# Performance work log

Measured on AMD Instinct MI355X. Metric: run time of the kernel, lower is better.

The kernel has to match this reference:

```python
import jax, jax.numpy as jnp
import numpy as np


def _ln(x, g, b, eps=1e-6):
    m = jnp.mean(x, axis=-1, keepdims=True)
    v = jnp.var(x, axis=-1, keepdims=True)
    return (x - m) * jax.lax.rsqrt(v + eps) * g + b


def setup_inputs():
    key = jax.random.key(0)
    ks = jax.random.split(key, 16)
    B, Hs, Ws, D = 2, 48, 48, 768
    heads, P = 6, 4
    L = Hs * Ws                # feat tokens (single level, 1/16 scale)
    N = 21 * (Hs * Ws // 4)    # query tokens: 16n + 4n + n multi-scale layout
    hidden = int(D * 0.25)
    s = 0.02
    return {
        "query": jax.random.normal(ks[0], (B, N, D), jnp.float32),
        "reference_points": jax.random.uniform(ks[1], (B, N, 1, 2), jnp.float32),
        "feat": jax.random.normal(ks[2], (B, L, D), jnp.float32),
        "spatial_shapes": jnp.array([[Hs, Ws]], jnp.int32),
        "level_start_index": jnp.array([0], jnp.int32),
        "H": Hs, "W": Ws,
        "qn_g": jnp.ones((D,), jnp.float32), "qn_b": jnp.zeros((D,), jnp.float32),
        "fn_g": jnp.ones((D,), jnp.float32), "fn_b": jnp.zeros((D,), jnp.float32),
        "Wv": jax.random.normal(ks[3], (D, D), jnp.float32) * s, "bv": jnp.zeros((D,), jnp.float32),
        "Woff": jax.random.normal(ks[4], (D, heads * P * 2), jnp.float32) * s,
        "boff": jax.random.normal(ks[5], (heads * P * 2,), jnp.float32) * s,
        "Wattn": jax.random.normal(ks[6], (D, heads * P), jnp.float32) * s,
        "battn": jnp.zeros((heads * P,), jnp.float32),
        "Wo": jax.random.normal(ks[7], (D, D), jnp.float32) * s, "bo": jnp.zeros((D,), jnp.float32),
        "ffn_g": jnp.ones((D,), jnp.float32), "ffn_b": jnp.zeros((D,), jnp.float32),
        "W1": jax.random.normal(ks[8], (D, hidden), jnp.float32) * s, "b1": jnp.zeros((hidden,), jnp.float32),
        "dw_w": jax.random.normal(ks[9], (hidden, 1, 3, 3), jnp.float32) * s, "dw_b": jnp.zeros((hidden,), jnp.float32),
        "W2": jax.random.normal(ks[10], (hidden, D), jnp.float32) * s, "b2": jnp.zeros((D,), jnp.float32),
    }


def reference(query, reference_points, feat, spatial_shapes, level_start_index, H, W,
              qn_g, qn_b, fn_g, fn_b, Wv, bv, Woff, boff, Wattn, battn, Wo, bo,
              ffn_g, ffn_b, W1, b1, dw_w, dw_b, W2, b2):
    B, N, D = query.shape
    heads, P = 6, 4
    dh = D // heads
    hidden = W1.shape[1]
    # ---- MSDeformAttn (single level) ----
    qn = _ln(query, qn_g, qn_b)
    fn = _ln(feat, fn_g, fn_b)
    value = (fn @ Wv + bv).reshape(B, -1, heads, dh)           # (B,L,h,dh)
    off = (qn @ Woff + boff).reshape(B, N, heads, 1, P, 2)
    aw = jax.nn.softmax((qn @ Wattn + battn).reshape(B, N, heads, P), axis=-1)
    # offset normalizer = [W_l, H_l]
    norm = jnp.stack([spatial_shapes[..., 1], spatial_shapes[..., 0]], -1).astype(qn.dtype)
    loc = reference_points[:, :, None, :, None, :] + off / norm[None, None, None, :, None, :]
    loc = loc[:, :, :, 0]  # (B,N,heads,P,2) single level
    # grid_sample bilinear, align_corners=False, zero padding
    x = loc[..., 0] * W - 0.5
    y = loc[..., 1] * H - 0.5
    x0 = jnp.floor(x); y0 = jnp.floor(y)
    wx = x - x0; wy = y - y0
    x0 = x0.astype(jnp.int32); y0 = y0.astype(jnp.int32)
    value_t = value.transpose(0, 2, 1, 3)  # (B,heads,L,dh)

    def corner(xi, yi, w):
        valid = (xi >= 0) & (xi < W) & (yi >= 0) & (yi < H)
        idx = jnp.clip(yi, 0, H - 1) * W + jnp.clip(xi, 0, W - 1)
        idx = idx.transpose(0, 2, 1, 3).reshape(B, heads, N * P)
        v = jnp.take_along_axis(value_t, idx[..., None], axis=2)  # (B,h,N*P,dh)
        wm = jnp.where(valid, w, 0.0).transpose(0, 2, 1, 3).reshape(B, heads, N * P)
        return v * wm[..., None]

    sampled = (corner(x0, y0, (1 - wx) * (1 - wy)) + corner(x0 + 1, y0, wx * (1 - wy))
               + corner(x0, y0 + 1, (1 - wx) * wy) + corner(x0 + 1, y0 + 1, wx * wy))
    sampled = sampled.reshape(B, heads, N, P, dh)
    attn = jnp.einsum('bhnpd,bnhp->bnhd', sampled, aw).reshape(B, N, D) @ Wo + bo
    query = query + attn
    # ---- ConvFFN (hidden=dim*cffn_ratio, multi-scale DWConv) ----
    h = _ln(query, ffn_g, ffn_b) @ W1 + b1
    n = N // 21

    def dw(t, hh, ww):
        img = t.transpose(0, 2, 1).reshape(B, hidden, hh, ww)
        out = jax.lax.conv_general_dilated(img, dw_w, (1, 1), 'SAME', feature_group_count=hidden)
        return (out + dw_b[None, :, None, None]).reshape(B, hidden, hh * ww).transpose(0, 2, 1)

    h = jnp.concatenate([dw(h[:, :16 * n], 2 * H, 2 * W),
                         dw(h[:, 16 * n:20 * n], H, W),
                         dw(h[:, 20 * n:], H // 2, W // 2)], axis=1)
    h = jax.nn.gelu(h, approximate=False)
    return query + (h @ W2 + b2)
```

## Files before the change

kernel.cpp:

```cpp
#include <hip/hip_runtime.h>
#include <math.h>

#define BB 2
#define NN 12096
#define LL 2304
#define DD 768
#define HID 192
#define HS 48
#define WS 48

typedef unsigned short u16;
typedef unsigned int u32;
typedef __attribute__((ext_vector_type(8))) __bf16 bf16x8;
typedef __attribute__((ext_vector_type(4))) float f32x4;

__device__ __forceinline__ u16 f2bf(float f) {
  u32 x = __builtin_bit_cast(u32, f);
  u32 r = (x + 0x7fffu + ((x >> 16) & 1u)) >> 16;
  return (u16)r;
}
__device__ __forceinline__ float bf2f(u16 u) {
  u32 x = ((u32)u) << 16;
  return __builtin_bit_cast(float, x);
}

template <typename T>
__device__ __forceinline__ void ln_row(const T* xr, const float* g, const float* bta, u16* yr, int t) {
  float v0, v1, v2;
  if constexpr (sizeof(T) == 2) {
    v0 = bf2f(xr[t]); v1 = bf2f(xr[t + 256]); v2 = bf2f(xr[t + 512]);
  } else {
    v0 = xr[t]; v1 = xr[t + 256]; v2 = xr[t + 512];
  }
  float s = v0 + v1 + v2;
  float s2 = v0 * v0 + v1 * v1 + v2 * v2;
#pragma unroll
  for (int off = 32; off; off >>= 1) {
    s += __shfl_down(s, off, 64);
    s2 += __shfl_down(s2, off, 64);
  }
  __shared__ float red[8];
  __shared__ float mv[2];
  int wave = t >> 6, lane = t & 63;
  if (lane == 0) { red[wave] = s; red[4 + wave] = s2; }
  __syncthreads();
  if (t == 0) {
    float ts = red[0] + red[1] + red[2] + red[3];
    float ts2 = red[4] + red[5] + red[6] + red[7];
    float m = ts * (1.f / DD);
    float var = ts2 * (1.f / DD) - m * m;
    mv[0] = m;
    mv[1] = rsqrtf(var + 1e-6f);
  }
  __syncthreads();
  float m = mv[0], rs = mv[1];
  yr[t]       = f2bf((v0 - m) * rs * g[t]       + bta[t]);
  yr[t + 256] = f2bf((v1 - m) * rs * g[t + 256] + bta[t + 256]);
  yr[t + 512] = f2bf((v2 - m) * rs * g[t + 512] + bta[t + 512]);
}

template <typename T>
__global__ __launch_bounds__(256) void ln_kernel(const T* __restrict__ x,
                                                 const float* __restrict__ g,
                                                 const float* __restrict__ bta,
                                                 u16* __restrict__ y) {
  size_t row = blockIdx.x;
  ln_row<T>(x + row * DD, g, bta, y + row * DD, threadIdx.x);
}

__global__ __launch_bounds__(256) void ln_dual_kernel(const float* __restrict__ xq,
                                                      const float* __restrict__ gq,
                                                      const float* __restrict__ bq,
                                                      u16* __restrict__ yq,
                                                      const float* __restrict__ xf,
                                                      const float* __restrict__ gf,
                                                      const float* __restrict__ bf_,
                                                      u16* __restrict__ yf,
                                                      int Mq) {
  size_t row = blockIdx.x;
  if (row < (size_t)Mq)
    ln_row<float>(xq + row * DD, gq, bq, yq + row * DD, threadIdx.x);
  else {
    size_t r = row - Mq;
    ln_row<float>(xf + r * DD, gf, bf_, yf + r * DD, threadIdx.x);
  }
}

template <int BM, int BN, int WM, int WN, int RES, int OUT, int NTSW>
__global__ __launch_bounds__(256, 2) void gemm_bf16(const u16* __restrict__ A,
                                                    const u16* __restrict__ Bt,
                                                    const float* __restrict__ bias,
                                                    const void* __restrict__ res,
                                                    void* __restrict__ Cv,
                                                    int M, int N, int K) {
  constexpr int PM = BM / WM, PN = BN / WN;
  constexpr int FM = PM / 16, FN = PN / 16;
  constexpr int ASEG = BM / 32;
  constexpr int BSEG = BN / 32;
  int bx, by;
  if (NTSW > 0) {
    int flat = blockIdx.x;
    int x = flat & 7, gidx = flat >> 3;
    bx = gidx % NTSW;
    int mg = gidx / NTSW;
    by = mg * 8 + x;
    if (by * BM >= M) return;
  } else {
    bx = blockIdx.x;
    by = blockIdx.y;
  }
  __shared__ u16 As[BM * 64];
  __shared__ u16 Bs[BN * 64];
  int tid = threadIdx.x;
  int w = tid >> 6, lane = tid & 63;
  int rw = w / WN, cw = w % WN;
  int m0 = by * BM, n0 = bx * BN;

  f32x4 acc[FM][FN];
#pragma unroll
  for (int i = 0; i < FM; ++i)
#pragma unroll
    for (int j = 0; j < FN; ++j) acc[i][j] = (f32x4){0.f, 0.f, 0.f, 0.f};

  int lr = lane >> 3;
  int lq = lane & 7;
  int qg = lq ^ lr;
  int l15 = lane & 15, quad = lane >> 4;

  for (int k0 = 0; k0 < K; k0 += 64) {
#pragma unroll
    for (int i = 0; i < ASEG; ++i) {
      int s = w * ASEG + i;
      int row = s * 8 + lr;
      const u16* gp = A + (size_t)(m0 + row) * K + k0 + qg * 8;
      __builtin_amdgcn_global_load_lds(
          (const __attribute__((address_space(1))) void*)gp,
          (__attribute__((address_space(3))) void*)&As[s * 512], 16, 0, 0);
    }
#pragma unroll
    for (int i = 0; i < BSEG; ++i) {
      int s = w * BSEG + i;
      int row = s * 8 + lr;
      const u16* gp = Bt + (size_t)(n0 + row) * K + k0 + qg * 8;
      __builtin_amdgcn_global_load_lds(
          (const __attribute__((address_space(1))) void*)gp,
          (__attribute__((address_space(3))) void*)&Bs[s * 512], 16, 0, 0);
    }
    __syncthreads();
#pragma unroll
    for (int s2 = 0; s2 < 2; ++s2) {
      bf16x8 af[FM], bfr[FN];
#pragma unroll
      for (int mt = 0; mt < FM; ++mt) {
        int rm = rw * PM + mt * 16 + l15;
        int ch = (s2 * 4 + quad) ^ (rm & 7);
        af[mt] = *(const bf16x8*)&As[rm * 64 + ch * 8];
      }
#pragma unroll
      for (int nt = 0; nt < FN; ++nt) {
        int rn = cw * PN + nt * 16 + l15;
        int ch = (s2 * 4 + quad) ^ (rn & 7);
        bfr[nt] = *(const bf16x8*)&Bs[rn * 64 + ch * 8];
      }
#pragma unroll
      for (int mt = 0; mt < FM; ++mt)
#pragma unroll
        for (int nt = 0; nt < FN; ++nt)
          acc[mt][nt] = __builtin_amdgcn_mfma_f32_16x16x32_bf16(af[mt], bfr[nt], acc[mt][nt], 0, 0, 0);
    }
    __syncthreads();
  }

#pragma unroll
  for (int mt = 0; mt < FM; ++mt) {
    int m = m0 + rw * PM + mt * 16 + quad * 4;
#pragma unroll
    for (int nt = 0; nt < FN; ++nt) {
      int n = n0 + cw * PN + nt * 16 + l15;
      float bsv = bias[n];
#pragma unroll
      for (int r = 0; r < 4; ++r) {
        size_t idx = (size_t)(m + r) * N + n;
        float v = acc[mt][nt][r] + bsv;
        if (RES == 1) v += ((const float*)res)[idx];
        if (RES == 2) v += bf2f(((const u16*)res)[idx]);
        if (OUT == 1) ((u16*)Cv)[idx] = f2bf(v);
        else ((float*)Cv)[idx] = v;
      }
    }
  }
}

#define PREP_B0 (DD * DD)
#define PREP_B1 (2 * DD * DD)
#define PREP_B2 (PREP_B1 + HID * DD)
#define PREP_B3 (PREP_B2 + HID * DD)
#define PREP_B4 (PREP_B3 + 128 * DD)
__global__ __launch_bounds__(256) void prep_all(const float* __restrict__ Wv, const float* __restrict__ Wo,
                                                const float* __restrict__ W1, const float* __restrict__ W2,
                                                const float* __restrict__ Woff, const float* __restrict__ Wattn,
                                                const float* __restrict__ boff, const float* __restrict__ battn,
                                                u16* __restrict__ Wv_t, u16* __restrict__ Wo_t,
                                                u16* __restrict__ W1_t, u16* __restrict__ W2_t,
                                                u16* __restrict__ Wcat_t, float* __restrict__ bias_cat) {
  int idx = blockIdx.x * 256 + threadIdx.x;
  if (idx >= PREP_B4) return;
  if (idx < PREP_B0) {
    int n = idx / DD, k = idx - n * DD;
    Wv_t[idx] = f2bf(Wv[(size_t)k * DD + n]);
  } else if (idx < PREP_B1) {
    int l = idx - PREP_B0;
    int n = l / DD, k = l - n * DD;
    Wo_t[l] = f2bf(Wo[(size_t)k * DD + n]);
  } else if (idx < PREP_B2) {
    int l = idx - PREP_B1;
    int n = l / DD, k = l - n * DD;
    W1_t[l] = f2bf(W1[(size_t)k * HID + n]);
  } else if (idx < PREP_B3) {
    int l = idx - PREP_B2;
    int n = l / HID, k = l - n * HID;
    W2_t[l] = f2bf(W2[(size_t)k * DD + n]);
  } else {
    int l = idx - PREP_B3;
    int n = l / DD, k = l - n * DD;
    float v = 0.f;
    if (n < 48) v = Woff[(size_t)k * 48 + n];
    else if (n < 72) v = Wattn[(size_t)k * 24 + (n - 48)];
    Wcat_t[l] = f2bf(v);
    if (l < 128) {
      float b = 0.f;
      if (l < 48) b = boff[l];
      else if (l < 72) b = battn[l - 48];
      bias_cat[l] = b;
    }
  }
}

__global__ __launch_bounds__(192) void sample_kernel(const u16* __restrict__ value,
                                                     const float* __restrict__ off,
                                                     const float* __restrict__ refp,
                                                     u16* __restrict__ s) {
  size_t row = blockIdx.x;
  int b = (int)(row / NN);
  __shared__ int cidx[96];
  __shared__ float cw[96];
  int t = threadIdx.x;
  if (t < 24) {
    const float* o = off + row * 128;
    int hh = t >> 2, p = t & 3;
    float l0 = o[48 + hh * 4 + 0], l1 = o[48 + hh * 4 + 1];
    float l2 = o[48 + hh * 4 + 2], l3 = o[48 + hh * 4 + 3];
    float mx = fmaxf(fmaxf(l0, l1), fmaxf(l2, l3));
    float e0 = expf(l0 - mx), e1 = expf(l1 - mx), e2 = expf(l2 - mx), e3 = expf(l3 - mx);
    float sum = e0 + e1 + e2 + e3;
    float et = (p == 0) ? e0 : (p == 1) ? e1 : (p == 2) ? e2 : e3;
    float aw = et / sum;
    float x = refp[row * 2 + 0] * (float)WS - 0.5f + o[hh * 8 + p * 2 + 0];
    float y = refp[row * 2 + 1] * (float)HS - 0.5f + o[hh * 8 + p * 2 + 1];
    float xf = floorf(x), yf = floorf(y);
    int x0 = (int)xf, y0 = (int)yf;
    float wx = x - xf, wy = y - yf;
#pragma unroll
    for (int c = 0; c < 4; ++c) {
      int xi = x0 + (c & 1), yi = y0 + (c >> 1);
      float w = ((c & 1) ? wx : 1.f - wx) * ((c >> 1) ? wy : 1.f - wy);
      bool valid = (xi >= 0) && (xi < WS) && (yi >= 0) && (yi < HS);
      int xc = min(max(xi, 0), WS - 1), yc = min(max(yi, 0), HS - 1);
      cidx[t * 4 + c] = yc * WS + xc;
      cw[t * 4 + c] = valid ? w * aw : 0.f;
    }
  }
  __syncthreads();
  const u16* vb = value + (size_t)b * LL * DD;
  int c = t * 4;
  int h = c >> 7;
  float a0 = 0.f, a1 = 0.f, a2 = 0.f, a3 = 0.f;
#pragma unroll
  for (int pp = 0; pp < 4; ++pp) {
    int base = (h * 4 + pp) * 4;
#pragma unroll
    for (int cc = 0; cc < 4; ++cc) {
      float w = cw[base + cc];
      ushort4 v = *(const ushort4*)&vb[(size_t)cidx[base + cc] * DD + c];
      a0 += w * bf2f(v.x);
      a1 += w * bf2f(v.y);
      a2 += w * bf2f(v.z);
      a3 += w * bf2f(v.w);
    }
  }
  ushort4 o4;
  o4.x = f2bf(a0); o4.y = f2bf(a1); o4.z = f2bf(a2); o4.w = f2bf(a3);
  *(ushort4*)&s[row * DD + c] = o4;
}

__global__ __launch_bounds__(256) void dwconv_gelu_kernel(const u16* __restrict__ h,
                                                          const float* __restrict__ w,
                                                          const float* __restrict__ bias,
                                                          u16* __restrict__ out) {
  size_t idx = (size_t)blockIdx.x * 256 + threadIdx.x;
  if (idx >= (size_t)BB * NN * HID) return;
  int c = (int)(idx % HID);
  int rem = (int)(idx / HID);
  int nidx = rem % NN;
  int b = rem / NN;
  int hh, ww, base;
  if (nidx < 9216)       { hh = 96; ww = 96; base = 0; }
  else if (nidx < 11520) { hh = 48; ww = 48; base = 9216; }
  else                   { hh = 24; ww = 24; base = 11520; }
  int p = nidx - base;
  int y = p / ww, x = p % ww;
  const u16* hb = h + ((size_t)b * NN + base) * HID;
  float acc = bias[c];
#pragma unroll
  for (int dy = -1; dy <= 1; ++dy) {
    int yy = y + dy;
    if (yy < 0 || yy >= hh) continue;
#pragma unroll
    for (int dx = -1; dx <= 1; ++dx) {
      int xx = x + dx;
      if (xx < 0 || xx >= ww) continue;
      acc += bf2f(hb[((size_t)(yy * ww + xx)) * HID + c]) * w[c * 9 + (dy + 1) * 3 + (dx + 1)];
    }
  }
  float g = 0.5f * acc * (1.f + erff(acc * 0.70710678118654752f));
  out[idx] = f2bf(g);
}

extern "C" void kernel_launch(void* const* d_in, const int* in_sizes, int n_in,
                              void* d_out, int out_size, void* d_ws, size_t ws_size,
                              hipStream_t stream) {
  const float* query = (const float*)d_in[0];
  const float* refp  = (const float*)d_in[1];
  const float* feat  = (const float*)d_in[2];
  const float* qn_g  = (const float*)d_in[7];
  const float* qn_b  = (const float*)d_in[8];
  const float* fn_g  = (const float*)d_in[9];
  const float* fn_b  = (const float*)d_in[10];
  const float* Wv    = (const float*)d_in[11];
  const float* bv    = (const float*)d_in[12];
  const float* Woff  = (const float*)d_in[13];
  const float* boff  = (const float*)d_in[14];
  const float* Wattn = (const float*)d_in[15];
  const float* battn = (const float*)d_in[16];
  const float* Wo    = (const float*)d_in[17];
  const float* bo    = (const float*)d_in[18];
  const float* ffn_g = (const float*)d_in[19];
  const float* ffn_b = (const float*)d_in[20];
  const float* W1    = (const float*)d_in[21];
  const float* b1    = (const float*)d_in[22];
  const float* dw_w  = (const float*)d_in[23];
  const float* dw_b  = (const float*)d_in[24];
  const float* W2    = (const float*)d_in[25];
  const float* b2    = (const float*)d_in[26];
  float* out = (float*)d_out;

  const int Mq = BB * NN;
  const int Mf = BB * LL;

  char* p = (char*)d_ws;
  auto alloc = [&](size_t bytes) { char* r = p; p += (bytes + 255) & ~(size_t)255; return r; };
  u16* qn_bf   = (u16*)alloc((size_t)Mq * DD * 2);
  u16* fn_bf   = (u16*)alloc((size_t)Mf * DD * 2);
  u16* val_bf  = (u16*)alloc((size_t)Mf * DD * 2);
  float* off   = (float*)alloc((size_t)Mq * 128 * 4);
  u16* s_bf    = (u16*)alloc((size_t)Mq * DD * 2);
  u16* q2_bf   = (u16*)alloc((size_t)Mq * DD * 2);
  u16* h_bf    = (u16*)alloc((size_t)Mq * HID * 2);
  u16* h2_bf   = (u16*)alloc((size_t)Mq * HID * 2);
  u16* Wv_t    = (u16*)alloc((size_t)DD * DD * 2);
  u16* Wo_t    = (u16*)alloc((size_t)DD * DD * 2);
  u16* W1_t    = (u16*)alloc((size_t)HID * DD * 2);
  u16* W2_t    = (u16*)alloc((size_t)DD * HID * 2);
  u16* Wcat_t  = (u16*)alloc((size_t)128 * DD * 2);
  float* bias_cat = (float*)alloc(128 * 4);

  prep_all<<<(PREP_B4 + 255) / 256, 256, 0, stream>>>(Wv, Wo, W1, W2, Woff, Wattn, boff, battn,
                                                      Wv_t, Wo_t, W1_t, W2_t, Wcat_t, bias_cat);

  ln_dual_kernel<<<Mq + Mf, 256, 0, stream>>>(query, qn_g, qn_b, qn_bf, feat, fn_g, fn_b, fn_bf, Mq);

  gemm_bf16<128, 128, 2, 2, 0, 1, 6><<<((Mf / 128 + 7) / 8) * 8 * 6, 256, 0, stream>>>(
      fn_bf, Wv_t, bv, nullptr, val_bf, Mf, DD, DD);

  gemm_bf16<64, 128, 2, 2, 0, 0, 0><<<dim3(1, Mq / 64), 256, 0, stream>>>(
      qn_bf, Wcat_t, bias_cat, nullptr, off, Mq, 128, DD);

  sample_kernel<<<Mq, 192, 0, stream>>>(val_bf, off, refp, s_bf);

  gemm_bf16<128, 128, 2, 2, 1, 1, 6><<<((Mq / 128 + 7) / 8) * 8 * 6, 256, 0, stream>>>(
      s_bf, Wo_t, bo, query, q2_bf, Mq, DD, DD);

  ln_kernel<u16><<<Mq, 256, 0, stream>>>(q2_bf, ffn_g, ffn_b, qn_bf);

  gemm_bf16<64, 192, 1, 4, 0, 1, 0><<<dim3(1, Mq / 64), 256, 0, stream>>>(
      qn_bf, W1_t, b1, nullptr, h_bf, Mq, HID, DD);

  {
    size_t total = (size_t)BB * NN * HID;
    int blocks = (int)((total + 255) / 256);
    dwconv_gelu_kernel<<<blocks, 256, 0, stream>>>(h_bf, dw_w, dw_b, h2_bf);
  }

  gemm_bf16<128, 128, 2, 2, 2, 0, 6><<<((Mq / 128 + 7) / 8) * 8 * 6, 256, 0, stream>>>(
      h2_bf, W2_t, b2, q2_bf, out, Mq, DD, HID);
}
```

Before: 413.2 us.

## Double-buffer GEMM LDS tiles and batch gather loads in deformable sampling

The GEMM kernel now keeps two LDS buffers and issues the global-to-LDS loads for the next K tile before computing on the current one, so memory latency overlaps with MFMA work and one barrier per iteration is removed. The sampling kernel first issues all 16 corner gathers into registers and only then accumulates, exposing more memory-level parallelism. In exchange, LDS use per block doubles, which can lower occupancy, and the gather adds register pressure.

```diff
diff --git a/kernel.cpp b/kernel.cpp
--- a/kernel.cpp
+++ b/kernel.cpp
@@ -109,8 +109,8 @@
     bx = blockIdx.x;
     by = blockIdx.y;
   }
-  __shared__ u16 As[BM * 64];
-  __shared__ u16 Bs[BN * 64];
+  __shared__ u16 As[2 * BM * 64];
+  __shared__ u16 Bs[2 * BN * 64];
   int tid = threadIdx.x;
   int w = tid >> 6, lane = tid & 63;
   int rw = w / WN, cw = w % WN;
@@ -127,26 +127,38 @@
   int qg = lq ^ lr;
   int l15 = lane & 15, quad = lane >> 4;
 
-  for (int k0 = 0; k0 < K; k0 += 64) {
+  int nk = K >> 6;
+
+  auto stage = [&](int kk, int buf) {
 #pragma unroll
     for (int i = 0; i < ASEG; ++i) {
       int s = w * ASEG + i;
       int row = s * 8 + lr;
-      const u16* gp = A + (size_t)(m0 + row) * K + k0 + qg * 8;
+      const u16* gp = A + (size_t)(m0 + row) * K + kk * 64 + qg * 8;
       __builtin_amdgcn_global_load_lds(
           (const __attribute__((address_space(1))) void*)gp,
-          (__attribute__((address_space(3))) void*)&As[s * 512], 16, 0, 0);
+          (__attribute__((address_space(3))) void*)&As[buf * (BM * 64) + s * 512], 16, 0, 0);
     }
 #pragma unroll
     for (int i = 0; i < BSEG; ++i) {
       int s = w * BSEG + i;
       int row = s * 8 + lr;
-      const u16* gp = Bt + (size_t)(n0 + row) * K + k0 + qg * 8;
+      const u16* gp = Bt + (size_t)(n0 + row) * K + kk * 64 + qg * 8;
       __builtin_amdgcn_global_load_lds(
           (const __attribute__((address_space(1))) void*)gp,
-          (__attribute__((address_space(3))) void*)&Bs[s * 512], 16, 0, 0);
-    }
-    __syncthreads();
+          (__attribute__((address_space(3))) void*)&Bs[buf * (BN * 64) + s * 512], 16, 0, 0);
+    }
+  };
+
+  stage(0, 0);
+  asm volatile("s_waitcnt vmcnt(0)" ::: "memory");
+  __builtin_amdgcn_s_barrier();
+
+  for (int t = 0; t < nk; ++t) {
+    int cur = t & 1;
+    if (t + 1 < nk) stage(t + 1, cur ^ 1);
+    const u16* Ab = As + cur * (BM * 64);
+    const u16* Bb = Bs + cur * (BN * 64);
 #pragma unroll
     for (int s2 = 0; s2 < 2; ++s2) {
       bf16x8 af[FM], bfr[FN];
@@ -154,13 +166,13 @@
       for (int mt = 0; mt < FM; ++mt) {
         int rm = rw * PM + mt * 16 + l15;
         int ch = (s2 * 4 + quad) ^ (rm & 7);
-        af[mt] = *(const bf16x8*)&As[rm * 64 + ch * 8];
+        af[mt] = *(const bf16x8*)&Ab[rm * 64 + ch * 8];
       }
 #pragma unroll
       for (int nt = 0; nt < FN; ++nt) {
         int rn = cw * PN + nt * 16 + l15;
         int ch = (s2 * 4 + quad) ^ (rn & 7);
-        bfr[nt] = *(const bf16x8*)&Bs[rn * 64 + ch * 8];
+        bfr[nt] = *(const bf16x8*)&Bb[rn * 64 + ch * 8];
       }
 #pragma unroll
       for (int mt = 0; mt < FM; ++mt)
@@ -168,7 +180,8 @@
         for (int nt = 0; nt < FN; ++nt)
           acc[mt][nt] = __builtin_amdgcn_mfma_f32_16x16x32_bf16(af[mt], bfr[nt], acc[mt][nt], 0, 0, 0);
     }
-    __syncthreads();
+    asm volatile("s_waitcnt vmcnt(0)" ::: "memory");
+    __builtin_amdgcn_s_barrier();
   }
 
 #pragma unroll
@@ -274,19 +287,19 @@
   const u16* vb = value + (size_t)b * LL * DD;
   int c = t * 4;
   int h = c >> 7;
+  int base0 = h * 16;
+  ushort4 v[16];
+#pragma unroll
+  for (int i = 0; i < 16; ++i)
+    v[i] = *(const ushort4*)&vb[(size_t)cidx[base0 + i] * DD + c];
   float a0 = 0.f, a1 = 0.f, a2 = 0.f, a3 = 0.f;
 #pragma unroll
-  for (int pp = 0; pp < 4; ++pp) {
-    int base = (h * 4 + pp) * 4;
-#pragma unroll
-    for (int cc = 0; cc < 4; ++cc) {
-      float w = cw[base + cc];
-      ushort4 v = *(const ushort4*)&vb[(size_t)cidx[base + cc] * DD + c];
-      a0 += w * bf2f(v.x);
-      a1 += w * bf2f(v.y);
-      a2 += w * bf2f(v.z);
-      a3 += w * bf2f(v.w);
-    }
+  for (int i = 0; i < 16; ++i) {
+    float w = cw[base0 + i];
+    a0 += w * bf2f(v[i].x);
+    a1 += w * bf2f(v[i].y);
+    a2 += w * bf2f(v[i].z);
+    a3 += w * bf2f(v[i].w);
   }
   ushort4 o4;
   o4.x = f2bf(a0); o4.y = f2bf(a1); o4.z = f2bf(a2); o4.w = f2bf(a3);
```

New measurement: 436.7 us. 5.7% more time.
